# Optimization experiments

Hardware: AMD Instinct MI355X
Metric: run time of the kernel (lower is better)

Reference implementation:

```python
import jax, jax.numpy as jnp
import numpy as np

# ---- Cl(3,0) Cayley table: blade order [1, e1, e2, e3, e12, e13, e23, e123] ----
_IDX2BM = [0, 1, 2, 4, 3, 5, 6, 7]
_BM2IDX = {b: i for i, b in enumerate(_IDX2BM)}

def _blade_mul(i, j):
    a, b = _IDX2BM[i], _IDX2BM[j]
    s, aa = 0, a >> 1
    while aa:
        s += bin(aa & b).count('1')
        aa >>= 1
    return _BM2IDX[a ^ b], (-1) ** s

_pairs = [(i, j) + _blade_mul(i, j) for i in range(8) for j in range(8) if i != j]
_pairs = [(i, j, k, s) for (i, j, k, s) in _pairs if k != i and k != j]
SRC_I = np.array([p[0] for p in _pairs])  # (42,)
SRC_J = np.array([p[1] for p in _pairs])
TGT   = np.array([p[2] for p in _pairs])
SIGN  = np.array([p[3] for p in _pairs], dtype=np.float32)

ROPE_THETA = 10000.0


def _rope_tables(T, D, dtype):
    inv_freq = 1.0 / (ROPE_THETA ** (jnp.arange(0, D, 2, dtype=jnp.float32) / D))
    freqs = jnp.arange(T, dtype=jnp.float32)[:, None] * inv_freq[None, :]  # (T, D/2)
    emb = jnp.concatenate([freqs, freqs], axis=-1)  # (T, D)
    return jnp.cos(emb).astype(dtype), jnp.sin(emb).astype(dtype)


def _rotate_half(x):
    x1, x2 = jnp.split(x, 2, axis=-1)
    return jnp.concatenate([-x2, x1], axis=-1)


def setup_inputs() -> dict:
    key = jax.random.key(0)
    k1, k2, k3 = jax.random.split(key, 3)
    B, T, N, D = 2, 2048, 8, 128
    d_model = N * D
    mv = jax.random.normal(k1, (B, T, N, D), dtype=jnp.float32)
    # nn.Linear weights, stored as (in, out) for x @ W; scaled like default init
    W_qkv = jax.random.normal(k2, (d_model, 3 * d_model), dtype=jnp.float32) / np.sqrt(d_model)
    W_o = jax.random.normal(k3, (d_model, d_model), dtype=jnp.float32) / np.sqrt(d_model)
    alpha = jnp.ones((8, 8), dtype=jnp.float32) * 0.01  # cayley_mix_init_scale
    return {"mv": mv, "W_qkv": W_qkv, "W_o": W_o, "alpha": alpha}


def reference(mv, W_qkv, W_o, alpha):
    B, T, N, D = mv.shape
    x_flat = mv.reshape(B, T, N * D)
    qkv = (x_flat @ W_qkv).reshape(B, T, 3, N, D)
    q, k, v = qkv[:, :, 0], qkv[:, :, 1], qkv[:, :, 2]  # (B, T, N, D)

    cos, sin = _rope_tables(T, D, mv.dtype)  # (T, D)
    cos = cos[None, :, None, :]
    sin = sin[None, :, None, :]
    q = q * cos + _rotate_half(q) * sin
    k = k * cos + _rotate_half(k) * sin

    # (B, N, T, D)
    q = q.transpose(0, 2, 1, 3)
    k = k.transpose(0, 2, 1, 3)
    v = v.transpose(0, 2, 1, 3)

    scale = 1.0 / jnp.sqrt(jnp.asarray(D, dtype=mv.dtype))
    scores = jnp.einsum('bntd,bnsd->bnts', q, k) * scale  # (B, N, T, T)
    causal = jnp.tril(jnp.ones((T, T), dtype=bool))
    scores = jnp.where(causal[None, None], scores, -jnp.inf)
    attn = jax.nn.softmax(scores, axis=-1)
    out = jnp.einsum('bnts,bnsd->bntd', attn, v)  # (B, N, T, D)

    out = out.transpose(0, 2, 1, 3).reshape(B, T, N * D)
    out = (out @ W_o).reshape(B, T, N, D)

    # Cayley cross-blade mixing
    si, sj, tgt = jnp.asarray(SRC_I), jnp.asarray(SRC_J), jnp.asarray(TGT)
    pair_w = alpha[si, sj] * jnp.asarray(SIGN)  # (42,)
    contrib = out[:, :, si, :] * out[:, :, sj, :] * pair_w[None, None, :, None]
    mixed = jnp.zeros_like(out).at[:, :, tgt, :].add(contrib)
    return out + mixed
```

## Files before the change

kernel.cpp:

```cpp
#include <hip/hip_runtime.h>
#include <stdint.h>


typedef __attribute__((ext_vector_type(8)))  __bf16 bf16x8;
typedef __attribute__((ext_vector_type(4)))  float  f32x4;

__device__ __forceinline__ uint16_t f2bf(float f) {
    uint32_t u = __float_as_uint(f);
    u += 0x7FFFu + ((u >> 16) & 1u);
    return (uint16_t)(u >> 16);
}
__device__ __forceinline__ float bf2f(uint16_t h) {
    return __uint_as_float(((uint32_t)h) << 16);
}

__device__ __forceinline__ void gload_lds16(const void* g, void* l) {
    __builtin_amdgcn_global_load_lds(
        (__attribute__((address_space(1))) void*)g,
        (__attribute__((address_space(3))) void*)l, 16, 0, 0);
}

__global__ __launch_bounds__(256) void k_prep(const float* __restrict__ mv,
                                              const float* __restrict__ Wqkv,
                                              const float* __restrict__ Wo,
                                              uint16_t* __restrict__ Xbf,
                                              uint16_t* __restrict__ Wqt,
                                              uint16_t* __restrict__ Wot,
                                              float* __restrict__ ct,
                                              float* __restrict__ st) {
    __shared__ uint16_t tile[64][65];
    const int bid = blockIdx.x;
    const int tid = threadIdx.x;
    if (bid < 4096) {
        int i = bid * 256 + tid;
        float4 v = ((const float4*)mv)[i];
        ((ushort4*)Xbf)[i] = make_ushort4(f2bf(v.x), f2bf(v.y), f2bf(v.z), f2bf(v.w));
    } else if (bid < 5120) {
        const float* W; uint16_t* Wt; int N, bx, by;
        if (bid < 4864) { W = Wqkv; Wt = Wqt; N = 3072;
                          int b2 = bid - 4096; bx = b2 % 48; by = b2 / 48; }
        else            { W = Wo;   Wt = Wot; N = 1024;
                          int b3 = bid - 4864; bx = b3 & 15; by = b3 >> 4; }
        const int k0 = by * 64, n0 = bx * 64;
        const int c = tid & 63, r4 = tid >> 6;
#pragma unroll
        for (int i = 0; i < 16; ++i) {
            int r = r4 + i * 4;
            tile[r][c] = f2bf(W[(size_t)(k0 + r) * N + n0 + c]);
        }
        __syncthreads();
#pragma unroll
        for (int i = 0; i < 16; ++i) {
            int r = r4 + i * 4;
            Wt[(size_t)(n0 + r) * 1024 + k0 + c] = tile[c][r];
        }
    } else {
        int i = (bid - 5120) * 256 + tid;
        int t = i >> 6, f = i & 63;
        float inv = expf(-(float)f * 0.14391156830441f);
        float ang = (float)t * inv;
        ct[i] = cosf(ang);
        st[i] = sinf(ang);
    }
}

__global__ __launch_bounds__(256) void k_gemmqkv(const uint16_t* __restrict__ A,
                                                 const uint16_t* __restrict__ Bt,
                                                 const float* __restrict__ ct,
                                                 const float* __restrict__ st,
                                                 uint16_t* __restrict__ Qr,
                                                 uint16_t* __restrict__ Kr,
                                                 uint16_t* __restrict__ Vt) {
    __shared__ __align__(16) char smem[33792];
    uint16_t* Atile = (uint16_t*)smem;
    uint16_t* Btile = (uint16_t*)(smem + 16384);
    const int lin = blockIdx.y * 24 + blockIdx.x;
    const int logical = (lin & 7) * 96 + (lin >> 3);
    const int bx = logical % 24;
    const int m0 = (logical / 24) << 7, n0 = bx << 7;
    const int sec = bx >> 3, head = bx & 7;
    const int tid = threadIdx.x;
    const int l = tid & 63, w = tid >> 6;
    const int lr = l & 15, lg = l >> 4;
    const int wm = (w >> 1) << 6, wn = (w & 1) << 6;
    const int K = 1024;

    f32x4 acc[4][4];
#pragma unroll
    for (int i = 0; i < 4; ++i)
#pragma unroll
        for (int j = 0; j < 4; ++j) acc[i][j] = (f32x4){0.f, 0.f, 0.f, 0.f};

    for (int kt = 0; kt < 16; ++kt) {
        const int k0 = kt << 6;
        __syncthreads();
#pragma unroll
        for (int c = 0; c < 8; ++c) {
            int idx = c * 256 + tid;
            if (idx < 1024) {
                int r = idx >> 3, c16 = idx & 7;
                int sc = c16 ^ (r & 7);
                gload_lds16(A + (size_t)(m0 + r) * K + k0 + sc * 8, Atile + idx * 8);
            } else {
                int i2 = idx - 1024;
                int r = i2 >> 3, c16 = i2 & 7;
                int sc = c16 ^ (r & 7);
                gload_lds16(Bt + (size_t)(n0 + r) * K + k0 + sc * 8, Btile + i2 * 8);
            }
        }
        __syncthreads();
#pragma unroll
        for (int kk = 0; kk < 2; ++kk) {
            bf16x8 af[4], bfv[4];
#pragma unroll
            for (int i = 0; i < 4; ++i) {
                int ra = wm + i * 16 + lr;
                af[i]  = *(const bf16x8*)((char*)Atile + ra * 128 +
                          ((kk * 64 + lg * 16) ^ ((ra & 7) << 4)));
                int rb = wn + i * 16 + lr;
                bfv[i] = *(const bf16x8*)((char*)Btile + rb * 128 +
                          ((kk * 64 + lg * 16) ^ ((rb & 7) << 4)));
            }
#pragma unroll
            for (int mi = 0; mi < 4; ++mi)
#pragma unroll
                for (int ni = 0; ni < 4; ++ni)
                    acc[mi][ni] = __builtin_amdgcn_mfma_f32_16x16x32_bf16(
                        af[mi], bfv[ni], acc[mi][ni], 0, 0, 0);
        }
    }

    __syncthreads();
    uint16_t (*Tl)[132] = (uint16_t(*)[132])smem;
#pragma unroll
    for (int mi = 0; mi < 4; ++mi)
#pragma unroll
        for (int ni = 0; ni < 4; ++ni)
#pragma unroll
            for (int r = 0; r < 4; ++r)
                Tl[wm + mi * 16 + lg * 4 + r][wn + ni * 16 + lr] =
                    f2bf(acc[mi][ni][r]);
    __syncthreads();

    const int b = m0 >> 11, t0 = m0 & 2047;
    const size_t hidx = (size_t)(b * 8 + head);
    if (sec < 2) {
        uint16_t* outp = (sec == 0 ? Qr : Kr) + (hidx * 2048 + t0) * 128;
#pragma unroll
        for (int it = 0; it < 8; ++it) {
            int lin2 = it * 256 + tid;
            int tr = lin2 >> 4, d0 = (lin2 & 15) * 4;
            ushort4 lo = *(const ushort4*)&Tl[tr][d0];
            ushort4 hi = *(const ushort4*)&Tl[tr][d0 + 64];
            float4 cv = *(const float4*)&ct[(size_t)(t0 + tr) * 64 + d0];
            float4 sv = *(const float4*)&st[(size_t)(t0 + tr) * 64 + d0];
            ushort4 o1, o2;
            o1.x = f2bf(bf2f(lo.x) * cv.x - bf2f(hi.x) * sv.x);
            o2.x = f2bf(bf2f(hi.x) * cv.x + bf2f(lo.x) * sv.x);
            o1.y = f2bf(bf2f(lo.y) * cv.y - bf2f(hi.y) * sv.y);
            o2.y = f2bf(bf2f(hi.y) * cv.y + bf2f(lo.y) * sv.y);
            o1.z = f2bf(bf2f(lo.z) * cv.z - bf2f(hi.z) * sv.z);
            o2.z = f2bf(bf2f(hi.z) * cv.z + bf2f(lo.z) * sv.z);
            o1.w = f2bf(bf2f(lo.w) * cv.w - bf2f(hi.w) * sv.w);
            o2.w = f2bf(bf2f(hi.w) * cv.w + bf2f(lo.w) * sv.w);
            *(ushort4*)&outp[(size_t)tr * 128 + d0]      = o1;
            *(ushort4*)&outp[(size_t)tr * 128 + d0 + 64] = o2;
        }
    } else {
        uint16_t* vp = Vt + hidx * 128 * 2048;
#pragma unroll
        for (int it = 0; it < 8; ++it) {
            int lin2 = it * 256 + tid;
            int d = lin2 >> 4, tq = (lin2 & 15) * 8;
            ushort4 v0 = make_ushort4(Tl[tq + 0][d], Tl[tq + 1][d],
                                      Tl[tq + 2][d], Tl[tq + 3][d]);
            ushort4 v1 = make_ushort4(Tl[tq + 4][d], Tl[tq + 5][d],
                                      Tl[tq + 6][d], Tl[tq + 7][d]);
            *(ushort4*)&vp[(size_t)d * 2048 + t0 + tq]     = v0;
            *(ushort4*)&vp[(size_t)d * 2048 + t0 + tq + 4] = v1;
        }
    }
}

__global__ __launch_bounds__(256) void k_gemm2s(const uint16_t* __restrict__ A,
                                                const uint16_t* __restrict__ Bt,
                                                float* __restrict__ C) {
    __shared__ uint16_t Atile[128 * 64];
    __shared__ uint16_t Btile[64 * 64];
    const int kz = blockIdx.z;
    A  += (size_t)kz * 512;
    Bt += (size_t)kz * 512;
    C  += (size_t)kz * (4096u * 1024u);
    const int lin = blockIdx.y * 16 + blockIdx.x;
    const int logical = (lin & 7) * 64 + (lin >> 3);
    const int m0 = (logical >> 4) << 7, n0 = (logical & 15) << 6;
    const int tid = threadIdx.x;
    const int l = tid & 63, w = tid >> 6;
    const int lr = l & 15, lg = l >> 4;
    const int wm = (w >> 1) << 6, wn = (w & 1) << 5;

    f32x4 acc[4][2];
#pragma unroll
    for (int i = 0; i < 4; ++i)
#pragma unroll
        for (int j = 0; j < 2; ++j) acc[i][j] = (f32x4){0.f, 0.f, 0.f, 0.f};

    for (int kt = 0; kt < 8; ++kt) {
        const int k0 = kt << 6;
        __syncthreads();
#pragma unroll
        for (int c = 0; c < 6; ++c) {
            int idx = c * 256 + tid;
            if (idx < 1024) {
                int r = idx >> 3, c16 = idx & 7;
                int sc = c16 ^ (r & 7);
                gload_lds16(A + (size_t)(m0 + r) * 1024 + k0 + sc * 8, Atile + idx * 8);
            } else {
                int i2 = idx - 1024;
                int r = i2 >> 3, c16 = i2 & 7;
                int sc = c16 ^ (r & 7);
                gload_lds16(Bt + (size_t)(n0 + r) * 1024 + k0 + sc * 8, Btile + i2 * 8);
            }
        }
        __syncthreads();
#pragma unroll
        for (int kk = 0; kk < 2; ++kk) {
            bf16x8 af[4], bfv[2];
#pragma unroll
            for (int i = 0; i < 4; ++i) {
                int ra = wm + i * 16 + lr;
                af[i] = *(const bf16x8*)((char*)Atile + ra * 128 +
                         ((kk * 64 + lg * 16) ^ ((ra & 7) << 4)));
            }
#pragma unroll
            for (int j = 0; j < 2; ++j) {
                int rb = wn + j * 16 + lr;
                bfv[j] = *(const bf16x8*)((char*)Btile + rb * 128 +
                          ((kk * 64 + lg * 16) ^ ((rb & 7) << 4)));
            }
#pragma unroll
            for (int mi = 0; mi < 4; ++mi)
#pragma unroll
                for (int ni = 0; ni < 2; ++ni)
                    acc[mi][ni] = __builtin_amdgcn_mfma_f32_16x16x32_bf16(
                        af[mi], bfv[ni], acc[mi][ni], 0, 0, 0);
        }
    }
#pragma unroll
    for (int mi = 0; mi < 4; ++mi)
#pragma unroll
        for (int ni = 0; ni < 2; ++ni)
#pragma unroll
            for (int r = 0; r < 4; ++r) {
                int row = m0 + wm + mi * 16 + lg * 4 + r;
                int col = n0 + wn + ni * 16 + lr;
                C[(size_t)row * 1024 + col] = acc[mi][ni][r];
            }
}

__global__ __launch_bounds__(256) void k_attn(const uint16_t* __restrict__ Qg,
                                              const uint16_t* __restrict__ Kg,
                                              const uint16_t* __restrict__ Vtg,
                                              uint16_t* __restrict__ AOg) {
    __shared__ uint16_t Klds[2][64 * 128];
    __shared__ uint16_t Vlds[2][128 * 64];
    __shared__ uint16_t Plds[4][16 * 64];

    const int bx = blockIdx.x;
    const int h  = bx & 15;
    const int t4 = (bx >> 4) & 15;
    const int qt = (bx < 256) ? (31 - t4) : t4;
    const int q0 = qt * 64;
    const int tid = threadIdx.x;
    const int l = tid & 63, w = tid >> 6;
    const int lr = l & 15, lg = l >> 4;
    const size_t headTD = (size_t)h * (2048 * 128);
    const uint16_t* Kh = Kg + headTD;
    const uint16_t* Vh = Vtg + headTD;

    bf16x8 qf[4];
    {
        const uint16_t* qp = Qg + headTD + (size_t)(q0 + w * 16 + lr) * 128 + lg * 8;
#pragma unroll
        for (int kc = 0; kc < 4; ++kc) qf[kc] = *(const bf16x8*)(qp + kc * 32);
    }

    f32x4 accO[8];
#pragma unroll
    for (int i = 0; i < 8; ++i) accO[i] = (f32x4){0.f, 0.f, 0.f, 0.f};
    float mrun = -1e30f, lrun = 0.f;

    const float SL2E = 0.08838834764831845f * 1.4426950408889634f;
    const int   swz  = (lr & 7) << 4;
    uint16_t* Pw = &Plds[w][0];

    auto STAGE = [&](int buf, int k0) {
#pragma unroll
        for (int p = 0; p < 4; ++p) {
            int u = p * 256 + tid;
            int row = u >> 4;
            int c16 = (u & 15) ^ (row & 7);
            gload_lds16(Kh + (size_t)(k0 + row) * 128 + c16 * 8,
                        (char*)&Klds[buf][0] + u * 16);
        }
#pragma unroll
        for (int p = 0; p < 4; ++p) {
            int u = p * 256 + tid;
            int d = u >> 3;
            int c8 = (u & 7) ^ (d & 7);
            gload_lds16(Vh + (size_t)d * 2048 + k0 + c8 * 8,
                        (char*)&Vlds[buf][0] + u * 16);
        }
    };

    STAGE(0, 0);

    for (int kt = 0; kt <= qt; ++kt) {
        asm volatile("s_waitcnt vmcnt(0)" ::: "memory");
        __builtin_amdgcn_s_barrier();
        __builtin_amdgcn_sched_barrier(0);
        if (kt < qt) STAGE((kt + 1) & 1, (kt + 1) * 64);

        const char* Kb = (const char*)&Klds[kt & 1][0];
        const char* Vb = (const char*)&Vlds[kt & 1][0];

        float sv[4][4];
        __builtin_amdgcn_s_setprio(1);
#pragma unroll
        for (int cg = 0; cg < 4; ++cg) {
            f32x4 a = (f32x4){0.f, 0.f, 0.f, 0.f};
#pragma unroll
            for (int kc = 0; kc < 4; ++kc) {
                int kb = (cg * 16 + lr) * 256 + ((kc * 64 + lg * 16) ^ swz);
                bf16x8 kf = *(const bf16x8*)(Kb + kb);
                a = __builtin_amdgcn_mfma_f32_16x16x32_bf16(kf, qf[kc], a, 0, 0, 0);
            }
#pragma unroll
            for (int r = 0; r < 4; ++r) sv[cg][r] = a[r];
        }
        __builtin_amdgcn_s_setprio(0);

        if (kt == qt) {
#pragma unroll
            for (int cg = 0; cg < 4; ++cg)
#pragma unroll
                for (int r = 0; r < 4; ++r)
                    if (cg * 16 + lg * 4 + r > w * 16 + lr) sv[cg][r] = -1e30f;
        }

        float pml = sv[0][0];
#pragma unroll
        for (int cg = 0; cg < 4; ++cg)
#pragma unroll
            for (int r = 0; r < 4; ++r) pml = fmaxf(pml, sv[cg][r]);

        if (!__all(pml * SL2E <= mrun + 11.f)) {
            float mx = pml;
            mx = fmaxf(mx, __shfl_xor(mx, 16, 64));
            mx = fmaxf(mx, __shfl_xor(mx, 32, 64));
            float mn = fmaxf(mrun, mx * SL2E);
            float corr = exp2f(mrun - mn);
            mrun = mn;
            lrun *= corr;
            float ca[4];
#pragma unroll
            for (int r = 0; r < 4; ++r)
                ca[r] = __shfl(corr, (lg << 4) + lg * 4 + r, 64);
#pragma unroll
            for (int i = 0; i < 8; ++i)
#pragma unroll
                for (int r = 0; r < 4; ++r) accO[i][r] *= ca[r];
        }

        float psum = 0.f;
        float p[4][4];
#pragma unroll
        for (int cg = 0; cg < 4; ++cg)
#pragma unroll
            for (int r = 0; r < 4; ++r) {
                p[cg][r] = exp2f(fmaf(sv[cg][r], SL2E, -mrun));
                psum += p[cg][r];
            }
        lrun += psum;

#pragma unroll
        for (int cg = 0; cg < 4; ++cg) {
            uint32_t w0, w1;
            asm("v_cvt_pk_bf16_f32 %0, %1, %2" : "=v"(w0) : "v"(p[cg][0]), "v"(p[cg][1]));
            asm("v_cvt_pk_bf16_f32 %0, %1, %2" : "=v"(w1) : "v"(p[cg][2]), "v"(p[cg][3]));
            uint2 pr; pr.x = w0; pr.y = w1;
            *(uint2*)((char*)Pw + lr * 128 + ((cg * 32 + lg * 8) ^ swz)) = pr;
        }

        asm volatile("" ::: "memory");
        bf16x8 pf[2];
#pragma unroll
        for (int c = 0; c < 2; ++c)
            pf[c] = *(const bf16x8*)((char*)Pw + lr * 128 + ((c * 64 + lg * 16) ^ swz));

        __builtin_amdgcn_s_setprio(1);
#pragma unroll
        for (int ni = 0; ni < 8; ++ni)
#pragma unroll
            for (int c = 0; c < 2; ++c) {
                int vb = (ni * 16 + lr) * 128 + ((c * 64 + lg * 16) ^ swz);
                bf16x8 vf = *(const bf16x8*)(Vb + vb);
                accO[ni] = __builtin_amdgcn_mfma_f32_16x16x32_bf16(pf[c], vf, accO[ni], 0, 0, 0);
            }
        __builtin_amdgcn_s_setprio(0);
    }

    float lsum = lrun;
    lsum += __shfl_xor(lsum, 16, 64);
    lsum += __shfl_xor(lsum, 32, 64);
    float linv = 1.f / lsum;
    float inv[4];
#pragma unroll
    for (int r = 0; r < 4; ++r)
        inv[r] = __shfl(linv, (lg << 4) + lg * 4 + r, 64);
    const int b = h >> 3, n = h & 7;
#pragma unroll
    for (int ni = 0; ni < 8; ++ni)
#pragma unroll
        for (int r = 0; r < 4; ++r) {
            int trow = q0 + w * 16 + lg * 4 + r;
            AOg[((size_t)(b * 2048 + trow)) * 1024 + n * 128 + ni * 16 + lr] =
                f2bf(accO[ni][r] * inv[r]);
        }
}

__global__ __launch_bounds__(256) void k_mix(const float* __restrict__ out0,
                                             const float* __restrict__ out1,
                                             const float* __restrict__ alpha,
                                             float* __restrict__ fin) {
    constexpr int SI[42] = {1,1,1,1,1,1, 2,2,2,2,2,2, 3,3,3,3,3,3, 4,4,4,4,4,4,
                            5,5,5,5,5,5, 6,6,6,6,6,6, 7,7,7,7,7,7};
    constexpr int SJ[42] = {2,3,4,5,6,7, 1,3,4,5,6,7, 1,2,4,5,6,7, 1,2,3,5,6,7,
                            1,2,3,4,6,7, 1,2,3,4,5,7, 1,2,3,4,5,6};
    constexpr int TG[42] = {4,5,2,3,7,6, 4,6,1,7,3,5, 5,6,7,1,2,4, 2,1,7,6,5,3,
                            3,7,1,6,4,2, 7,3,2,5,4,1, 6,5,4,3,2,1};
    constexpr float SG[42] = {+1,+1,+1,+1,+1,+1, -1,+1,-1,-1,+1,-1, -1,-1,+1,-1,-1,+1,
                              -1,+1,+1,-1,+1,-1, -1,-1,+1,+1,-1,+1, +1,-1,+1,-1,+1,-1,
                              +1,-1,+1,-1,+1,-1};
    int idx = blockIdx.x * 256 + threadIdx.x;
    int dq = (idx & 31) * 4, bt = idx >> 5;
    size_t base = (size_t)bt * 1024 + dq;
    float4 o[8], r[8];
#pragma unroll
    for (int hh = 0; hh < 8; ++hh) {
        float4 a = *(const float4*)&out0[base + hh * 128];
        float4 b = *(const float4*)&out1[base + hh * 128];
        o[hh] = make_float4(a.x + b.x, a.y + b.y, a.z + b.z, a.w + b.w);
        r[hh] = o[hh];
    }
#pragma unroll
    for (int p = 0; p < 42; ++p) {
        float wgt = alpha[SI[p] * 8 + SJ[p]] * SG[p];
        r[TG[p]].x += wgt * o[SI[p]].x * o[SJ[p]].x;
        r[TG[p]].y += wgt * o[SI[p]].y * o[SJ[p]].y;
        r[TG[p]].z += wgt * o[SI[p]].z * o[SJ[p]].z;
        r[TG[p]].w += wgt * o[SI[p]].w * o[SJ[p]].w;
    }
#pragma unroll
    for (int hh = 0; hh < 8; ++hh) *(float4*)&fin[base + hh * 128] = r[hh];
}

extern "C" void kernel_launch(void* const* d_in, const int* in_sizes, int n_in,
                              void* d_out, int out_size, void* d_ws, size_t ws_size,
                              hipStream_t stream) {
    (void)in_sizes; (void)n_in; (void)out_size; (void)ws_size;
    const float* mv    = (const float*)d_in[0];
    const float* Wqkv  = (const float*)d_in[1];
    const float* Wo    = (const float*)d_in[2];
    const float* alpha = (const float*)d_in[3];
    float* outp = (float*)d_out;
    char* ws = (char*)d_ws;

    uint16_t* Xbf  = (uint16_t*)(ws + 0);
    uint16_t* Wqt  = (uint16_t*)(ws + 8388608);
    uint16_t* Wot  = (uint16_t*)(ws + 14680064);
    uint16_t* Qr   = (uint16_t*)(ws + 41943040);
    uint16_t* Kr   = (uint16_t*)(ws + 50331648);
    uint16_t* Vt   = (uint16_t*)(ws + 58720256);
    float*    ctab = (float*)(ws + 67108864);
    float*    stab = (float*)(ws + 67633152);
    uint16_t* AO   = (uint16_t*)(ws + 0);
    float*    outF0 = (float*)(ws + 16777216);
    float*    outF1 = (float*)(ws + 33554432);

    k_prep   <<<5632, 256, 0, stream>>>(mv, Wqkv, Wo, Xbf, Wqt, Wot, ctab, stab);
    k_gemmqkv<<<dim3(24, 32), 256, 0, stream>>>(Xbf, Wqt, ctab, stab, Qr, Kr, Vt);
    k_attn   <<<512, 256, 0, stream>>>(Qr, Kr, Vt, AO);
    k_gemm2s <<<dim3(16, 32, 2), 256, 0, stream>>>(AO, Wot, outF0);
    k_mix    <<<512, 256, 0, stream>>>(outF0, outF1, alpha, outp);
}
```

Measured before the change: 121.5 us.

## Split causal attention KV range into chunks and merge partials in separate kernel

Attention work is split along the key dimension into chunks of up to 8 KV tiles, giving 1280 blocks instead of 512. Each block writes an unnormalized bf16 partial output plus its running max and sum, and a new merge kernel combines the partials with log-sum-exp rescaling. This targets load imbalance and the long tail from the causal triangle, since the longest rows no longer dominate. In exchange it adds a kernel launch, extra global traffic for partials, and bf16 rounding of unnormalized partials, and it reuses workspace regions that other kernels also use.

```diff
diff --git a/kernel.cpp b/kernel.cpp
--- a/kernel.cpp
+++ b/kernel.cpp
@@ -3,6 +3,7 @@
 
 
 typedef __attribute__((ext_vector_type(8)))  __bf16 bf16x8;
+typedef __attribute__((ext_vector_type(8)))  uint16_t u16x8;
 typedef __attribute__((ext_vector_type(4)))  float  f32x4;
 
 __device__ __forceinline__ uint16_t f2bf(float f) {
@@ -261,15 +262,22 @@
 __global__ __launch_bounds__(256) void k_attn(const uint16_t* __restrict__ Qg,
                                               const uint16_t* __restrict__ Kg,
                                               const uint16_t* __restrict__ Vtg,
-                                              uint16_t* __restrict__ AOg) {
+                                              uint16_t* __restrict__ pbuf,
+                                              float* __restrict__ mlg) {
     __shared__ uint16_t Klds[2][64 * 128];
     __shared__ uint16_t Vlds[2][128 * 64];
     __shared__ uint16_t Plds[4][16 * 64];
 
-    const int bx = blockIdx.x;
-    const int h  = bx & 15;
-    const int t4 = (bx >> 4) & 15;
-    const int qt = (bx < 256) ? (31 - t4) : t4;
+    const int h = blockIdx.x;
+    int sy = blockIdx.y, qt = 31, ci = 0;
+    for (int q = 31; q >= 0; --q) {
+        int nc = (q + 8) >> 3;
+        if (sy < nc) { qt = q; ci = sy; break; }
+        sy -= nc;
+    }
+    const int slot = h * 80 + blockIdx.y;
+    const int p0 = ci * 8;
+    const int pend = min(p0 + 8, qt + 1);
     const int q0 = qt * 64;
     const int tid = threadIdx.x;
     const int l = tid & 63, w = tid >> 6;
@@ -313,13 +321,13 @@
         }
     };
 
-    STAGE(0, 0);
-
-    for (int kt = 0; kt <= qt; ++kt) {
+    STAGE(0, p0 * 64);
+
+    for (int kt = p0; kt < pend; ++kt) {
         asm volatile("s_waitcnt vmcnt(0)" ::: "memory");
         __builtin_amdgcn_s_barrier();
         __builtin_amdgcn_sched_barrier(0);
-        if (kt < qt) STAGE((kt + 1) & 1, (kt + 1) * 64);
+        if (kt + 1 < pend) STAGE((kt + 1) & 1, (kt + 1) * 64);
 
         const char* Kb = (const char*)&Klds[kt & 1][0];
         const char* Vb = (const char*)&Vlds[kt & 1][0];
@@ -413,20 +421,60 @@
     float lsum = lrun;
     lsum += __shfl_xor(lsum, 16, 64);
     lsum += __shfl_xor(lsum, 32, 64);
-    float linv = 1.f / lsum;
-    float inv[4];
-#pragma unroll
-    for (int r = 0; r < 4; ++r)
-        inv[r] = __shfl(linv, (lg << 4) + lg * 4 + r, 64);
+    uint16_t* pb = pbuf + (size_t)slot * 8192;
+#pragma unroll
+    for (int ni = 0; ni < 8; ++ni)
+#pragma unroll
+        for (int r = 0; r < 4; ++r) {
+            int row = w * 16 + lg * 4 + r;
+            pb[row * 128 + ni * 16 + lr] = f2bf(accO[ni][r]);
+        }
+    if (lg == 0) {
+        mlg[slot * 128 + w * 16 + lr]      = mrun;
+        mlg[slot * 128 + 64 + w * 16 + lr] = lsum;
+    }
+}
+
+__global__ __launch_bounds__(256) void k_amerge(const uint16_t* __restrict__ pbuf,
+                                                const float* __restrict__ mlg,
+                                                uint16_t* __restrict__ AOg) {
+    const int h = blockIdx.x, qt = blockIdx.y;
+    int base = 0;
+    for (int q = 31; q > qt; --q) base += (q + 8) >> 3;
+    const int nc = (qt + 8) >> 3;
+    const int slot0 = h * 80 + base;
+    const int tid = threadIdx.x;
+    const int row = tid >> 2, dq = (tid & 3) * 32;
+
+    float M = -1e30f;
+    for (int ci = 0; ci < nc; ++ci)
+        M = fmaxf(M, mlg[(slot0 + ci) * 128 + row]);
+    float L = 0.f;
+    float o[32];
+#pragma unroll
+    for (int j = 0; j < 32; ++j) o[j] = 0.f;
+    for (int ci = 0; ci < nc; ++ci) {
+        int sl = slot0 + ci;
+        float wgt = exp2f(mlg[sl * 128 + row] - M);
+        L += mlg[sl * 128 + 64 + row] * wgt;
+        const u16x8* pv = (const u16x8*)(pbuf + (size_t)sl * 8192 + row * 128 + dq);
+#pragma unroll
+        for (int jj = 0; jj < 4; ++jj) {
+            u16x8 v = pv[jj];
+#pragma unroll
+            for (int k = 0; k < 8; ++k) o[jj * 8 + k] += bf2f(v[k]) * wgt;
+        }
+    }
+    float inv = 1.f / L;
     const int b = h >> 3, n = h & 7;
-#pragma unroll
-    for (int ni = 0; ni < 8; ++ni)
-#pragma unroll
-        for (int r = 0; r < 4; ++r) {
-            int trow = q0 + w * 16 + lg * 4 + r;
-            AOg[((size_t)(b * 2048 + trow)) * 1024 + n * 128 + ni * 16 + lr] =
-                f2bf(accO[ni][r] * inv[r]);
-        }
+    uint16_t* op = AOg + ((size_t)(b * 2048 + qt * 64 + row)) * 1024 + n * 128 + dq;
+#pragma unroll
+    for (int jj = 0; jj < 4; ++jj) {
+        u16x8 v;
+#pragma unroll
+        for (int k = 0; k < 8; ++k) v[k] = f2bf(o[jj * 8 + k] * inv);
+        ((u16x8*)op)[jj] = v;
+    }
 }
 
 __global__ __launch_bounds__(256) void k_mix(const float* __restrict__ out0,
@@ -485,12 +533,15 @@
     float*    ctab = (float*)(ws + 67108864);
     float*    stab = (float*)(ws + 67633152);
     uint16_t* AO   = (uint16_t*)(ws + 0);
+    float*    mlg  = (float*)(ws + 8388608);
+    uint16_t* pbuf = (uint16_t*)(ws + 16777216);
     float*    outF0 = (float*)(ws + 16777216);
     float*    outF1 = (float*)(ws + 33554432);
 
     k_prep   <<<5632, 256, 0, stream>>>(mv, Wqkv, Wo, Xbf, Wqt, Wot, ctab, stab);
     k_gemmqkv<<<dim3(24, 32), 256, 0, stream>>>(Xbf, Wqt, ctab, stab, Qr, Kr, Vt);
-    k_attn   <<<512, 256, 0, stream>>>(Qr, Kr, Vt, AO);
+    k_attn   <<<dim3(16, 80), 256, 0, stream>>>(Qr, Kr, Vt, pbuf, mlg);
+    k_amerge <<<dim3(16, 32), 256, 0, stream>>>(pbuf, mlg, AO);
     k_gemm2s <<<dim3(16, 32, 2), 256, 0, stream>>>(AO, Wot, outF0);
     k_mix    <<<512, 256, 0, stream>>>(outF0, outF1, alpha, outp);
 }
```

Result: no change. 123.9 us (+2.0%).
